# Performance work log

Hardware: AMD Instinct MI355X
Metric: run time of the kernel (lower is better)

Reference implementation:

```python
import jax, jax.numpy as jnp
import numpy as np

N, E, G = 20000, 320000, 64
IN_DIM, HID, HEADS, NCLS = 512, 256, 2, 10
EPS = 1e-5
SLOPE = 0.2


def setup_inputs() -> dict:
    key = jax.random.key(0)
    ks = jax.random.split(key, 24)
    s = 0.02
    inp = {
        "feat": jax.random.normal(ks[0], (N, IN_DIM), jnp.float32),
        "src": jax.random.randint(ks[1], (E,), 0, N, jnp.int32),
        "dst": jax.random.randint(ks[2], (E,), 0, N, jnp.int32),
        "graph_ids": jnp.sort(jax.random.randint(ks[3], (N,), 0, G, jnp.int32)),
        # GATv2Conv params (fc_src, fc_dst, attn)
        "W_src": jax.random.normal(ks[4], (IN_DIM, HEADS * HID), jnp.float32) * s,
        "b_src": jnp.zeros((HEADS * HID,), jnp.float32),
        "W_dst": jax.random.normal(ks[5], (IN_DIM, HEADS * HID), jnp.float32) * s,
        "b_dst": jnp.zeros((HEADS * HID,), jnp.float32),
        "attn": jax.random.normal(ks[6], (HEADS, HID), jnp.float32) * s,
        # skip_lin: input_dim -> 2*hidden
        "W_skip": jax.random.normal(ks[7], (IN_DIM, 2 * HID), jnp.float32) * s,
        "b_skip": jnp.zeros((2 * HID,), jnp.float32),
        # bn1 affine
        "gamma": jnp.ones((2 * HID,), jnp.float32),
        "beta": jnp.zeros((2 * HID,), jnp.float32),
        # dim_reducer
        "W_red": jax.random.normal(ks[8], (2 * HID, HID), jnp.float32) * s,
        "b_red": jnp.zeros((HID,), jnp.float32),
        # attention-pool gate Linear(hidden, 1)
        "w_gate": jax.random.normal(ks[9], (HID, 1), jnp.float32) * s,
        "b_gate": jnp.zeros((1,), jnp.float32),
        # classifier MLP
        "W1": jax.random.normal(ks[10], (HID, HID // 2), jnp.float32) * s,
        "b1": jnp.zeros((HID // 2,), jnp.float32),
        "W2": jax.random.normal(ks[11], (HID // 2, NCLS), jnp.float32) * s,
        "b2": jnp.zeros((NCLS,), jnp.float32),
    }
    return inp


def _gatv2(feat, src, dst, W_src, b_src, W_dst, b_dst, attn):
    # feat_src/feat_dst: [N, H, D]
    fs = (feat @ W_src + b_src).reshape(N, HEADS, HID)
    fd = (feat @ W_dst + b_dst).reshape(N, HEADS, HID)
    fs_e = fs[src]                               # [E, H, D]
    m = jax.nn.leaky_relu(fs_e + fd[dst], SLOPE)  # [E, H, D]
    e = jnp.einsum("ehd,hd->eh", m, attn)         # [E, H]
    # edge softmax grouped by destination node
    e_max = jax.ops.segment_max(e, dst, num_segments=N)          # [N, H]
    e_exp = jnp.exp(e - e_max[dst])                               # [E, H]
    denom = jax.ops.segment_sum(e_exp, dst, num_segments=N)      # [N, H]
    alpha = e_exp / denom[dst]                                    # [E, H]
    out = jax.ops.segment_sum(alpha[:, :, None] * fs_e, dst, num_segments=N)
    return out  # [N, H, D]; zero rows for zero in-degree nodes


def reference(feat, src, dst, graph_ids, W_src, b_src, W_dst, b_dst, attn,
              W_skip, b_skip, gamma, beta, W_red, b_red, w_gate, b_gate,
              W1, b1, W2, b2):
    h1 = jax.nn.elu(_gatv2(feat, src, dst, W_src, b_src, W_dst, b_dst, attn))
    h1 = h1.reshape(N, HEADS * HID)
    h1 = h1 + (feat @ W_skip + b_skip)
    # BatchNorm1d (training-mode batch statistics, biased variance)
    mu = jnp.mean(h1, axis=0)
    var = jnp.mean((h1 - mu) ** 2, axis=0)
    h1 = (h1 - mu) * jax.lax.rsqrt(var + EPS) * gamma + beta
    hr = h1 @ W_red + b_red                      # [N, HID]
    # GlobalAttentionPooling: segment softmax of gate scores over each graph
    gate = hr @ w_gate + b_gate                  # [N, 1]
    g_max = jax.ops.segment_max(gate, graph_ids, num_segments=G)
    g_exp = jnp.exp(gate - g_max[graph_ids])
    g_den = jax.ops.segment_sum(g_exp, graph_ids, num_segments=G)
    a = g_exp / g_den[graph_ids]                 # [N, 1]
    h_g = jax.ops.segment_sum(a * hr, graph_ids, num_segments=G)  # [G, HID]
    # classifier (dropout = identity at inference)
    return jax.nn.relu(h_g @ W1 + b1) @ W2 + b2  # [G, NCLS]
```

## Files before the change

kernel.cpp:

```cpp
#include <hip/hip_runtime.h>
#include <math.h>

#define N_NODES 20000
#define N_EDGES 320000
#define N_GRAPH 64
#define IN_DIM  512
#define HID     256
#define F2      512
#define EPS_BN  1e-5f
#define SLOPE   0.2f
#define SCAN_BLOCKS 79
#define N_RT    157
#define RT_PAD  20096

typedef unsigned short u16;
typedef __attribute__((ext_vector_type(8))) short bf16x8;
typedef __attribute__((ext_vector_type(4))) float floatx4;

__device__ __forceinline__ u16 bf_hi(float x) {
    unsigned int u = __float_as_uint(x);
    return (u16)((u + 0x7fffu + ((u >> 16) & 1u)) >> 16);
}
__device__ __forceinline__ float bf_val(u16 h) {
    return __uint_as_float((unsigned int)h << 16);
}
__device__ __forceinline__ void unpack2(unsigned int u, float& lo, float& hi) {
    lo = __uint_as_float(u << 16);
    hi = __uint_as_float(u & 0xffff0000u);
}
__device__ __forceinline__ float lr(float x) { return fmaxf(x, SLOPE * x); }

__global__ void init_zero_kernel(int* counts, int* cursor, float* stats,
                                 float* h_gnum, float* gden) {
    int i = blockIdx.x * blockDim.x + threadIdx.x;
    if (i < N_NODES) { counts[i] = 0; cursor[i] = 0; }
    if (i < 1024) stats[i] = 0.f;
    if (i < N_GRAPH * HID) h_gnum[i] = 0.f;
    if (i < N_GRAPH) gden[i] = 0.f;
}

__global__ __launch_bounds__(256) void split_feat_kernel(
    const float* __restrict__ X, u16* __restrict__ Hi, int total8, int pad8) {
    int i = blockIdx.x * 256 + threadIdx.x;
    if (i >= pad8) return;
    size_t base = (size_t)i * 8;
    if (i >= total8) {
        *(uint4*)(Hi + base) = make_uint4(0, 0, 0, 0);
        return;
    }
    float4 x0 = *(const float4*)(X + base);
    float4 x1 = *(const float4*)(X + base + 4);
    float xs[8] = {x0.x, x0.y, x0.z, x0.w, x1.x, x1.y, x1.z, x1.w};
    union { u16 s[8]; uint4 v; } h;
#pragma unroll
    for (int j = 0; j < 8; j++) h.s[j] = bf_hi(xs[j]);
    *(uint4*)(Hi + base) = h.v;
}

__global__ __launch_bounds__(256) void split_wt_kernel(
    const float* __restrict__ Ws, const float* __restrict__ Wd,
    const float* __restrict__ Wk, const float* __restrict__ Wr,
    u16* __restrict__ Hi, u16* __restrict__ Lo) {
    __shared__ float t[32][33];
    int w = blockIdx.z;
    int ncols = (w == 3) ? 256 : 512;
    int n0 = blockIdx.y * 32;
    if (n0 >= ncols) return;
    const float* W = (w == 0) ? Ws : ((w == 1) ? Wd : ((w == 2) ? Wk : Wr));
    size_t obase = (size_t)w * 512 * 512;
    int k0 = blockIdx.x * 32;
    int tx = threadIdx.x, ty = threadIdx.y;
#pragma unroll
    for (int i = 0; i < 4; i++)
        t[ty * 4 + i][tx] = W[(size_t)(k0 + ty * 4 + i) * ncols + n0 + tx];
    __syncthreads();
#pragma unroll
    for (int i = 0; i < 4; i++) {
        float x = t[tx][ty * 4 + i];
        u16 hh = bf_hi(x);
        size_t o = obase + (size_t)(n0 + ty * 4 + i) * 512 + k0 + tx;
        Hi[o] = hh;
        Lo[o] = bf_hi(x - bf_val(hh));
    }
}

__global__ __launch_bounds__(256) void gemm_mfma_triple(
    const u16* __restrict__ Fhi, const u16* __restrict__ Wthi,
    const float* __restrict__ b_src, const float* __restrict__ b_dst,
    const float* __restrict__ b_skip,
    u16* __restrict__ FS16, u16* __restrict__ FD16, float* __restrict__ h1) {
    __shared__ u16 As[2][128 * 72];
    int b = blockIdx.x;
    int xcd = b & 7, slot = b >> 3;
    int rt = (slot / 12) * 8 + xcd;
    if (rt >= N_RT) return;
    int cw = slot % 12;
    int w_idx = cw >> 2;
    int col0 = (cw & 3) * 128;
    int row0 = rt * 128;
    int tid = threadIdx.x;
    int lane = tid & 63, wave = tid >> 6;
    int wm = (wave & 1) * 64, wn = (wave >> 1) * 64;
    int quad = lane >> 4, l16 = lane & 15;

    int sr = tid >> 1, sh = (tid & 1) * 32;
    const u16* gA = Fhi + (size_t)(row0 + sr) * 512 + sh;
    int sOff = sr * 72 + sh;

    const u16* Wb = Wthi + (size_t)w_idx * 512 * 512;
    const u16* bP[4];
#pragma unroll
    for (int nt = 0; nt < 4; nt++)
        bP[nt] = Wb + (size_t)(col0 + wn + nt * 16 + l16) * 512 + quad * 8;

    floatx4 acc[4][4];
#pragma unroll
    for (int i = 0; i < 4; i++)
#pragma unroll
        for (int j = 0; j < 4; j++) acc[i][j] = (floatx4){0.f, 0.f, 0.f, 0.f};

    union { uint4 u; bf16x8 v; } bcur[8], bnxt[8];
    {
        uint4 a0 = *(const uint4*)(gA + 0);
        uint4 a1 = *(const uint4*)(gA + 8);
        uint4 a2 = *(const uint4*)(gA + 16);
        uint4 a3 = *(const uint4*)(gA + 24);
#pragma unroll
        for (int nt = 0; nt < 4; nt++) {
            bcur[nt * 2 + 0].u = *(const uint4*)(bP[nt] + 0);
            bcur[nt * 2 + 1].u = *(const uint4*)(bP[nt] + 32);
        }
        *(uint4*)(&As[0][sOff + 0])  = a0;
        *(uint4*)(&As[0][sOff + 8])  = a1;
        *(uint4*)(&As[0][sOff + 16]) = a2;
        *(uint4*)(&As[0][sOff + 24]) = a3;
    }
    __syncthreads();

    for (int kk = 0; kk < 8; kk++) {
        uint4 na0, na1, na2, na3;
        bool more = kk < 7;
        if (more) {
            int k1 = (kk + 1) * 64;
            na0 = *(const uint4*)(gA + k1 + 0);
            na1 = *(const uint4*)(gA + k1 + 8);
            na2 = *(const uint4*)(gA + k1 + 16);
            na3 = *(const uint4*)(gA + k1 + 24);
#pragma unroll
            for (int nt = 0; nt < 4; nt++) {
                bnxt[nt * 2 + 0].u = *(const uint4*)(bP[nt] + k1 + 0);
                bnxt[nt * 2 + 1].u = *(const uint4*)(bP[nt] + k1 + 32);
            }
        }
        const u16* base = &As[kk & 1][0];
#pragma unroll
        for (int s = 0; s < 2; s++) {
#pragma unroll
            for (int mt = 0; mt < 4; mt++) {
                bf16x8 ah = *(const bf16x8*)&base[(wm + mt * 16 + l16) * 72 + s * 32 + quad * 8];
#pragma unroll
                for (int nt = 0; nt < 4; nt++)
                    acc[mt][nt] = __builtin_amdgcn_mfma_f32_16x16x32_bf16(ah, bcur[nt * 2 + s].v, acc[mt][nt], 0, 0, 0);
            }
        }
        if (more) {
            u16* d = &As[(kk + 1) & 1][sOff];
            *(uint4*)(d + 0)  = na0;
            *(uint4*)(d + 8)  = na1;
            *(uint4*)(d + 16) = na2;
            *(uint4*)(d + 24) = na3;
            __syncthreads();
#pragma unroll
            for (int i = 0; i < 8; i++) bcur[i] = bnxt[i];
        }
    }

    const float* bias = (w_idx == 0) ? b_src : ((w_idx == 1) ? b_dst : b_skip);
    float bv[4];
#pragma unroll
    for (int nt = 0; nt < 4; nt++) bv[nt] = bias[col0 + wn + nt * 16 + l16];
#pragma unroll
    for (int mt = 0; mt < 4; mt++) {
#pragma unroll
        for (int r = 0; r < 4; r++) {
            int m = row0 + wm + mt * 16 + quad * 4 + r;
            if (m < N_NODES) {
#pragma unroll
                for (int nt = 0; nt < 4; nt++) {
                    int n = col0 + wn + nt * 16 + l16;
                    float vv = acc[mt][nt][r] + bv[nt];
                    if (w_idx == 0)      FS16[(size_t)m * 512 + n] = bf_hi(vv);
                    else if (w_idx == 1) FD16[(size_t)m * 512 + n] = bf_hi(vv);
                    else                 h1[(size_t)m * 512 + n] = vv;
                }
            }
        }
    }
}

__global__ __launch_bounds__(256) void gemm_mfma_red(
    const float* __restrict__ Af,
    const u16* __restrict__ Bhi, const u16* __restrict__ Blo,
    const float* __restrict__ bias, float* __restrict__ C,
    int Nrows, int M,
    const float* __restrict__ bscale, const float* __restrict__ bshift) {
    __shared__ u16 AsHi[128 * 40];
    __shared__ u16 AsLo[128 * 40];
    __shared__ float sBN[1024];
    int tid = threadIdx.x;
    int row0 = blockIdx.x * 128;
    int col0 = blockIdx.y * 128;
    int lane = tid & 63, wave = tid >> 6;
    int wm = (wave & 1) * 64, wn = (wave >> 1) * 64;
    int quad = lane >> 4, l16 = lane & 15;

    sBN[tid] = bscale[tid]; sBN[256 + tid] = bscale[256 + tid];
    sBN[512 + tid] = bshift[tid]; sBN[768 + tid] = bshift[256 + tid];
    __syncthreads();

    int sr = tid >> 1, sh = (tid & 1) * 16;
    int grow = row0 + sr;
    bool ok = grow < Nrows;
    u16* sA_hi = &AsHi[sr * 40 + sh];
    u16* sA_lo = &AsLo[sr * 40 + sh];

    floatx4 acc[4][4];
#pragma unroll
    for (int i = 0; i < 4; i++)
#pragma unroll
        for (int j = 0; j < 4; j++) acc[i][j] = (floatx4){0.f, 0.f, 0.f, 0.f};

    for (int k0 = 0; k0 < 512; k0 += 32) {
        float v[16];
        if (ok) {
            const float* g = Af + (size_t)grow * 512 + k0 + sh;
            *(float4*)&v[0]  = *(const float4*)(g);
            *(float4*)&v[4]  = *(const float4*)(g + 4);
            *(float4*)&v[8]  = *(const float4*)(g + 8);
            *(float4*)&v[12] = *(const float4*)(g + 12);
        } else {
#pragma unroll
            for (int j = 0; j < 16; j++) v[j] = 0.f;
        }
        union { u16 s[8]; uint4 u; } h0_, h1_, l0_, l1_;
#pragma unroll
        for (int j = 0; j < 16; j++) {
            int kc = k0 + sh + j;
            float x = v[j] * sBN[kc] + sBN[512 + kc];
            u16 hh = bf_hi(x);
            u16 ll = bf_hi(x - bf_val(hh));
            if (j < 8) { h0_.s[j] = hh; l0_.s[j] = ll; }
            else       { h1_.s[j - 8] = hh; l1_.s[j - 8] = ll; }
        }
        union { uint4 u; bf16x8 v; } bh[4], bl[4];
#pragma unroll
        for (int nt = 0; nt < 4; nt++) {
            size_t off = (size_t)(col0 + wn + nt * 16 + l16) * 512 + k0 + quad * 8;
            bh[nt].u = *(const uint4*)(Bhi + off);
            bl[nt].u = *(const uint4*)(Blo + off);
        }
        __syncthreads();
        *(uint4*)(sA_hi + 0) = h0_.u;
        *(uint4*)(sA_hi + 8) = h1_.u;
        *(uint4*)(sA_lo + 0) = l0_.u;
        *(uint4*)(sA_lo + 8) = l1_.u;
        __syncthreads();
#pragma unroll
        for (int mt = 0; mt < 4; mt++) {
            int me = (wm + mt * 16 + l16) * 40 + quad * 8;
            bf16x8 ah = *(const bf16x8*)&AsHi[me];
            bf16x8 al = *(const bf16x8*)&AsLo[me];
#pragma unroll
            for (int nt = 0; nt < 4; nt++) {
                acc[mt][nt] = __builtin_amdgcn_mfma_f32_16x16x32_bf16(ah, bh[nt].v, acc[mt][nt], 0, 0, 0);
                acc[mt][nt] = __builtin_amdgcn_mfma_f32_16x16x32_bf16(ah, bl[nt].v, acc[mt][nt], 0, 0, 0);
                acc[mt][nt] = __builtin_amdgcn_mfma_f32_16x16x32_bf16(al, bh[nt].v, acc[mt][nt], 0, 0, 0);
            }
        }
    }

    float bv[4];
#pragma unroll
    for (int nt = 0; nt < 4; nt++) bv[nt] = bias[col0 + wn + nt * 16 + l16];
#pragma unroll
    for (int mt = 0; mt < 4; mt++) {
#pragma unroll
        for (int r = 0; r < 4; r++) {
            int m = row0 + wm + mt * 16 + quad * 4 + r;
            if (m < Nrows) {
#pragma unroll
                for (int nt = 0; nt < 4; nt++) {
                    int n = col0 + wn + nt * 16 + l16;
                    C[(size_t)m * M + n] = acc[mt][nt][r] + bv[nt];
                }
            }
        }
    }
}

__global__ void hist_kernel(const int* __restrict__ dst, int* __restrict__ counts) {
    int e = blockIdx.x * blockDim.x + threadIdx.x;
    if (e < N_EDGES) atomicAdd(&counts[dst[e]], 1);
}

__global__ __launch_bounds__(256) void scan_local_kernel(
    const int* __restrict__ counts, int* __restrict__ row_ptr, int* __restrict__ bsum) {
    __shared__ int buf[256];
    int b = blockIdx.x, tid = threadIdx.x;
    int i = b * 256 + tid;
    buf[tid] = (i < N_NODES) ? counts[i] : 0;
    __syncthreads();
    for (int off = 1; off < 256; off <<= 1) {
        int t = (tid >= off) ? buf[tid - off] : 0;
        __syncthreads();
        buf[tid] += t;
        __syncthreads();
    }
    if (i < N_NODES) row_ptr[i + 1] = buf[tid];
    if (tid == 255) bsum[b] = buf[255];
}

__global__ __launch_bounds__(256) void scan_fixup_kernel(
    const int* __restrict__ bsum, int* __restrict__ row_ptr) {
    __shared__ int red[256];
    int b = blockIdx.x, tid = threadIdx.x;
    red[tid] = (tid < b) ? bsum[tid] : 0;
    __syncthreads();
    for (int off = 128; off > 0; off >>= 1) {
        if (tid < off) red[tid] += red[tid + off];
        __syncthreads();
    }
    int offset = red[0];
    int i = b * 256 + tid;
    if (i < N_NODES) row_ptr[i + 1] += offset;
    if (b == 0 && tid == 0) row_ptr[0] = 0;
}

__global__ void scatter_kernel(const int* __restrict__ src, const int* __restrict__ dst,
                               const int* __restrict__ row_ptr,
                               int* __restrict__ cursor, int* __restrict__ csr_src) {
    int e = blockIdx.x * blockDim.x + threadIdx.x;
    if (e < N_EDGES) {
        int d = dst[e];
        int pos = atomicAdd(&cursor[d], 1);
        csr_src[row_ptr[d] + pos] = src[e];
    }
}

__global__ __launch_bounds__(256) void edge_fused_kernel(
    const u16* __restrict__ FS16, const u16* __restrict__ FD16,
    const float* __restrict__ attn, const int* __restrict__ csr_src,
    const int* __restrict__ row_ptr, float* __restrict__ h1) {
    __shared__ float red[3 * 512];
    __shared__ float den[2];
    int n = blockIdx.x, tid = threadIdx.x;
    int lane = tid & 63, wave = tid >> 6;
    int beg = row_ptr[n], end = row_ptr[n + 1], deg = end - beg;
    if (tid < 2) den[tid] = 0.f;

    float fdv[8], aw[8];
    {
        uint4 q = *(const uint4*)(FD16 + (size_t)n * 512 + 8 * lane);
        unpack2(q.x, fdv[0], fdv[1]); unpack2(q.y, fdv[2], fdv[3]);
        unpack2(q.z, fdv[4], fdv[5]); unpack2(q.w, fdv[6], fdv[7]);
        float4 a0 = *(const float4*)(attn + 8 * lane);
        float4 a1 = *(const float4*)(attn + 8 * lane + 4);
        aw[0] = a0.x; aw[1] = a0.y; aw[2] = a0.z; aw[3] = a0.w;
        aw[4] = a1.x; aw[5] = a1.y; aw[6] = a1.z; aw[7] = a1.w;
    }
    __syncthreads();

    float acc[8] = {0.f, 0.f, 0.f, 0.f, 0.f, 0.f, 0.f, 0.f};
    float dp = 0.f;
    for (int j = wave; j < deg; j += 4) {
        int s = csr_src[beg + j];
        uint4 q = *(const uint4*)(FS16 + (size_t)s * 512 + 8 * lane);
        float f[8];
        unpack2(q.x, f[0], f[1]); unpack2(q.y, f[2], f[3]);
        unpack2(q.z, f[4], f[5]); unpack2(q.w, f[6], f[7]);
        float p = 0.f;
#pragma unroll
        for (int k = 0; k < 8; k++) p += lr(f[k] + fdv[k]) * aw[k];
#pragma unroll
        for (int off = 16; off > 0; off >>= 1) p += __shfl_xor(p, off, 64);
        float ex = expf(p);
#pragma unroll
        for (int k = 0; k < 8; k++) acc[k] += ex * f[k];
        if ((lane & 31) == 0) dp += ex;
    }
    if ((lane & 31) == 0) atomicAdd(&den[lane >> 5], dp);

    if (wave > 0) {
        float* r = &red[(wave - 1) * 512 + lane * 8];
        *(float4*)(r + 0) = *(float4*)&acc[0];
        *(float4*)(r + 4) = *(float4*)&acc[4];
    }
    __syncthreads();
    if (wave == 0) {
#pragma unroll
        for (int w = 0; w < 3; w++) {
            const float* r = &red[w * 512 + lane * 8];
#pragma unroll
            for (int k = 0; k < 8; k++) acc[k] += r[k];
        }
        float d = (lane < 32) ? den[0] : den[1];
        float inv = d > 0.f ? 1.f / d : 0.f;
        float* hp = h1 + (size_t)n * 512 + 8 * lane;
        float4 s0 = *(float4*)(hp);
        float4 s1 = *(float4*)(hp + 4);
        float v[8];
#pragma unroll
        for (int k = 0; k < 8; k++) {
            float x = acc[k] * inv;
            v[k] = x > 0.f ? x : expm1f(x);
        }
        s0.x += v[0]; s0.y += v[1]; s0.z += v[2]; s0.w += v[3];
        s1.x += v[4]; s1.y += v[5]; s1.z += v[6]; s1.w += v[7];
        *(float4*)(hp) = s0;
        *(float4*)(hp + 4) = s1;
    }
}

__global__ __launch_bounds__(256) void bn_stats_kernel(const float* __restrict__ h1,
                                                       float* __restrict__ stats,
                                                       int rows_per_block) {
    int tid = threadIdx.x;
    int r0 = blockIdx.x * rows_per_block;
    int r1 = min(r0 + rows_per_block, N_NODES);
    float s0 = 0.f, q0 = 0.f, s1 = 0.f, q1 = 0.f;
    for (int r = r0; r < r1; r++) {
        float a = h1[(size_t)r * F2 + tid];
        float b = h1[(size_t)r * F2 + 256 + tid];
        s0 += a; q0 += a * a;
        s1 += b; q1 += b * b;
    }
    atomicAdd(&stats[tid], s0);
    atomicAdd(&stats[256 + tid], s1);
    atomicAdd(&stats[512 + tid], q0);
    atomicAdd(&stats[512 + 256 + tid], q1);
}

__global__ void bn_finalize_kernel(const float* __restrict__ stats,
                                   const float* __restrict__ gamma,
                                   const float* __restrict__ beta,
                                   float* __restrict__ bscale, float* __restrict__ bshift) {
    int c = threadIdx.x;
    float mu = stats[c] / (float)N_NODES;
    float var = stats[512 + c] / (float)N_NODES - mu * mu;
    float sc = gamma[c] * rsqrtf(var + EPS_BN);
    bscale[c] = sc;
    bshift[c] = beta[c] - mu * sc;
}

__global__ __launch_bounds__(256) void gate_kernel(const float* __restrict__ hr,
                                                   const float* __restrict__ wg,
                                                   float* __restrict__ gate) {
    int n = blockIdx.x * 4 + (threadIdx.x >> 6);
    int lane = threadIdx.x & 63;
    const float4* row = (const float4*)(hr + (size_t)n * HID);
    const float4* w = (const float4*)wg;
    float4 a = row[lane], b = w[lane];
    float p = a.x * b.x + a.y * b.y + a.z * b.z + a.w * b.w;
#pragma unroll
    for (int off = 32; off > 0; off >>= 1) p += __shfl_down(p, off, 64);
    if (lane == 0) gate[n] = p;
}

__device__ __forceinline__ int lower_bound_dev(const int* a, int n, int v) {
    int lo = 0, hi = n;
    while (lo < hi) {
        int mid = (lo + hi) >> 1;
        if (a[mid] < v) lo = mid + 1; else hi = mid;
    }
    return lo;
}

__global__ __launch_bounds__(256) void pool_partial_kernel(
    const float* __restrict__ hr, const float* __restrict__ gate,
    const int* __restrict__ gids, float* __restrict__ h_gnum,
    float* __restrict__ gden) {
    int b = blockIdx.x;
    int g = b >> 3, part = b & 7;
    int tid = threadIdx.x;
    int start = lower_bound_dev(gids, N_NODES, g);
    int end = lower_bound_dev(gids, N_NODES, g + 1);
    int span = end - start;
    int p_beg = start + (span * part) / 8;
    int p_end = start + (span * (part + 1)) / 8;
    if (p_beg >= p_end) return;
    __shared__ float wa[256];
    __shared__ float red[256];
    float acc = 0.f, denacc = 0.f;
    for (int cbeg = p_beg; cbeg < p_end; cbeg += 256) {
        int c = min(256, p_end - cbeg);
        float e = 0.f;
        if (tid < c) { e = expf(gate[cbeg + tid]); wa[tid] = e; }
        red[tid] = (tid < c) ? e : 0.f;
        __syncthreads();
        for (int off = 128; off > 0; off >>= 1) {
            if (tid < off) red[tid] += red[tid + off];
            __syncthreads();
        }
        denacc += red[0];
        for (int i = 0; i < c; i++) acc += wa[i] * hr[(size_t)(cbeg + i) * HID + tid];
        __syncthreads();
    }
    atomicAdd(&h_gnum[g * HID + tid], acc);
    if (tid == 0) atomicAdd(&gden[g], denacc);
}

__global__ __launch_bounds__(128) void classifier_kernel(
    const float* __restrict__ h_gnum, const float* __restrict__ gden,
    const float* __restrict__ W1, const float* __restrict__ b1,
    const float* __restrict__ W2, const float* __restrict__ b2,
    float* __restrict__ out) {
    int g = blockIdx.x;
    int tid = threadIdx.x;
    __shared__ float hg[256];
    __shared__ float z1[128];
    float d = gden[g];
    float invd = d > 0.f ? 1.f / d : 0.f;
    hg[tid] = h_gnum[g * HID + tid] * invd;
    hg[tid + 128] = h_gnum[g * HID + tid + 128] * invd;
    __syncthreads();
    float a = b1[tid];
#pragma unroll 8
    for (int k = 0; k < 256; k++) a += hg[k] * W1[k * 128 + tid];
    z1[tid] = a > 0.f ? a : 0.f;
    __syncthreads();
    if (tid < 10) {
        float o = b2[tid];
#pragma unroll 8
        for (int j = 0; j < 128; j++) o += z1[j] * W2[j * 10 + tid];
        out[g * 10 + tid] = o;
    }
}

extern "C" void kernel_launch(void* const* d_in, const int* in_sizes, int n_in,
                              void* d_out, int out_size, void* d_ws, size_t ws_size,
                              hipStream_t stream) {
    const float* feat   = (const float*)d_in[0];
    const int*   src    = (const int*)d_in[1];
    const int*   dst    = (const int*)d_in[2];
    const int*   gids   = (const int*)d_in[3];
    const float* W_src  = (const float*)d_in[4];
    const float* b_src  = (const float*)d_in[5];
    const float* W_dst  = (const float*)d_in[6];
    const float* b_dst  = (const float*)d_in[7];
    const float* attn   = (const float*)d_in[8];
    const float* W_skip = (const float*)d_in[9];
    const float* b_skip = (const float*)d_in[10];
    const float* gamma  = (const float*)d_in[11];
    const float* beta   = (const float*)d_in[12];
    const float* W_red  = (const float*)d_in[13];
    const float* b_red  = (const float*)d_in[14];
    const float* w_gate = (const float*)d_in[15];
    const float* W1     = (const float*)d_in[17];
    const float* b1     = (const float*)d_in[18];
    const float* W2     = (const float*)d_in[19];
    const float* b2     = (const float*)d_in[20];
    float* out = (float*)d_out;

    char* p = (char*)d_ws;
    auto alloc = [&](size_t bytes) -> char* {
        char* r = p;
        p += (bytes + 255) & ~(size_t)255;
        return r;
    };
    u16*   FS16     = (u16*)alloc((size_t)N_NODES * F2 * 2);
    u16*   FD16     = (u16*)alloc((size_t)N_NODES * F2 * 2);
    float* h1       = (float*)alloc((size_t)N_NODES * F2 * 4);
    float* gate     = (float*)alloc((size_t)N_NODES * 4);
    float* stats    = (float*)alloc(1024 * 4);
    float* bn_scale = (float*)alloc(512 * 4);
    float* bn_shift = (float*)alloc(512 * 4);
    float* h_gnum   = (float*)alloc((size_t)N_GRAPH * HID * 4);
    float* gden     = (float*)alloc((size_t)N_GRAPH * 4);
    int* counts     = (int*)alloc((size_t)N_NODES * 4);
    int* row_ptr    = (int*)alloc((size_t)(N_NODES + 1) * 4);
    int* cursor     = (int*)alloc((size_t)N_NODES * 4);
    int* csr_src    = (int*)alloc((size_t)N_EDGES * 4);
    int* bsum       = (int*)alloc((size_t)SCAN_BLOCKS * 4);
    u16* Fhi        = (u16*)alloc((size_t)RT_PAD * IN_DIM * 2);
    u16* Wthi       = (u16*)alloc((size_t)4 * 512 * 512 * 2);
    u16* Wtlo       = (u16*)alloc((size_t)4 * 512 * 512 * 2);
    float* hr = (float*)Fhi;
    (void)ws_size; (void)in_sizes; (void)n_in; (void)out_size;

    const size_t WSZ = (size_t)512 * 512;

    init_zero_kernel<<<(N_NODES + 255) / 256, 256, 0, stream>>>(counts, cursor, stats, h_gnum, gden);
    split_feat_kernel<<<(RT_PAD * IN_DIM / 8 + 255) / 256, 256, 0, stream>>>(
        feat, Fhi, N_NODES * IN_DIM / 8, RT_PAD * IN_DIM / 8);
    split_wt_kernel<<<dim3(16, 16, 4), dim3(32, 8), 0, stream>>>(
        W_src, W_dst, W_skip, W_red, Wthi, Wtlo);

    gemm_mfma_triple<<<dim3(((N_RT + 7) / 8) * 8 * 12), 256, 0, stream>>>(
        Fhi, Wthi, b_src, b_dst, b_skip, FS16, FD16, h1);

    hist_kernel<<<(N_EDGES + 255) / 256, 256, 0, stream>>>(dst, counts);
    scan_local_kernel<<<SCAN_BLOCKS, 256, 0, stream>>>(counts, row_ptr, bsum);
    scan_fixup_kernel<<<SCAN_BLOCKS, 256, 0, stream>>>(bsum, row_ptr);
    scatter_kernel<<<(N_EDGES + 255) / 256, 256, 0, stream>>>(src, dst, row_ptr, cursor, csr_src);

    edge_fused_kernel<<<N_NODES, 256, 0, stream>>>(FS16, FD16, attn, csr_src, row_ptr, h1);

    bn_stats_kernel<<<500, 256, 0, stream>>>(h1, stats, 40);
    bn_finalize_kernel<<<1, 512, 0, stream>>>(stats, gamma, beta, bn_scale, bn_shift);

    dim3 g256((N_NODES + 127) / 128, 2);
    gemm_mfma_red<<<g256, 256, 0, stream>>>(
        h1, Wthi + 3 * WSZ, Wtlo + 3 * WSZ, b_red, hr, N_NODES, HID,
        bn_scale, bn_shift);

    gate_kernel<<<N_NODES / 4, 256, 0, stream>>>(hr, w_gate, gate);

    pool_partial_kernel<<<N_GRAPH * 8, 256, 0, stream>>>(hr, gate, gids, h_gnum, gden);

    classifier_kernel<<<N_GRAPH, 128, 0, stream>>>(h_gnum, gden, W1, b1, W2, b2, out);
}
```

Before: 423.5 us.

## Store h1 as bf16 hi/lo pairs, fold BN into W_red, fuse gate into GEMM

The skip/h1 buffer is now kept as split bf16 hi/lo halves instead of fp32, and the edge kernel does its read-modify-write in that format. BatchNorm scale and shift are folded into the reduction weights and bias by a new small kernel, so the reduction GEMM loads pre-split A tiles with no per-element conversion. The gate dot product moves into the GEMM epilogue through shuffles and atomics, which removes one kernel and a reread of hr. BN statistics are computed from the hi half only, which slightly lowers their precision.

```diff
diff --git a/kernel.cpp b/kernel.cpp
--- a/kernel.cpp
+++ b/kernel.cpp
@@ -31,9 +31,9 @@
 __device__ __forceinline__ float lr(float x) { return fmaxf(x, SLOPE * x); }
 
 __global__ void init_zero_kernel(int* counts, int* cursor, float* stats,
-                                 float* h_gnum, float* gden) {
+                                 float* h_gnum, float* gden, float* gate) {
     int i = blockIdx.x * blockDim.x + threadIdx.x;
-    if (i < N_NODES) { counts[i] = 0; cursor[i] = 0; }
+    if (i < N_NODES) { counts[i] = 0; cursor[i] = 0; gate[i] = 0.f; }
     if (i < 1024) stats[i] = 0.f;
     if (i < N_GRAPH * HID) h_gnum[i] = 0.f;
     if (i < N_GRAPH) gden[i] = 0.f;
@@ -88,7 +88,8 @@
     const u16* __restrict__ Fhi, const u16* __restrict__ Wthi,
     const float* __restrict__ b_src, const float* __restrict__ b_dst,
     const float* __restrict__ b_skip,
-    u16* __restrict__ FS16, u16* __restrict__ FD16, float* __restrict__ h1) {
+    u16* __restrict__ FS16, u16* __restrict__ FD16,
+    u16* __restrict__ h1hi, u16* __restrict__ h1lo) {
     __shared__ u16 As[2][128 * 72];
     int b = blockIdx.x;
     int xcd = b & 7, slot = b >> 3;
@@ -191,107 +192,11 @@
                     float vv = acc[mt][nt][r] + bv[nt];
                     if (w_idx == 0)      FS16[(size_t)m * 512 + n] = bf_hi(vv);
                     else if (w_idx == 1) FD16[(size_t)m * 512 + n] = bf_hi(vv);
-                    else                 h1[(size_t)m * 512 + n] = vv;
-                }
-            }
-        }
-    }
-}
-
-__global__ __launch_bounds__(256) void gemm_mfma_red(
-    const float* __restrict__ Af,
-    const u16* __restrict__ Bhi, const u16* __restrict__ Blo,
-    const float* __restrict__ bias, float* __restrict__ C,
-    int Nrows, int M,
-    const float* __restrict__ bscale, const float* __restrict__ bshift) {
-    __shared__ u16 AsHi[128 * 40];
-    __shared__ u16 AsLo[128 * 40];
-    __shared__ float sBN[1024];
-    int tid = threadIdx.x;
-    int row0 = blockIdx.x * 128;
-    int col0 = blockIdx.y * 128;
-    int lane = tid & 63, wave = tid >> 6;
-    int wm = (wave & 1) * 64, wn = (wave >> 1) * 64;
-    int quad = lane >> 4, l16 = lane & 15;
-
-    sBN[tid] = bscale[tid]; sBN[256 + tid] = bscale[256 + tid];
-    sBN[512 + tid] = bshift[tid]; sBN[768 + tid] = bshift[256 + tid];
-    __syncthreads();
-
-    int sr = tid >> 1, sh = (tid & 1) * 16;
-    int grow = row0 + sr;
-    bool ok = grow < Nrows;
-    u16* sA_hi = &AsHi[sr * 40 + sh];
-    u16* sA_lo = &AsLo[sr * 40 + sh];
-
-    floatx4 acc[4][4];
-#pragma unroll
-    for (int i = 0; i < 4; i++)
-#pragma unroll
-        for (int j = 0; j < 4; j++) acc[i][j] = (floatx4){0.f, 0.f, 0.f, 0.f};
-
-    for (int k0 = 0; k0 < 512; k0 += 32) {
-        float v[16];
-        if (ok) {
-            const float* g = Af + (size_t)grow * 512 + k0 + sh;
-            *(float4*)&v[0]  = *(const float4*)(g);
-            *(float4*)&v[4]  = *(const float4*)(g + 4);
-            *(float4*)&v[8]  = *(const float4*)(g + 8);
-            *(float4*)&v[12] = *(const float4*)(g + 12);
-        } else {
-#pragma unroll
-            for (int j = 0; j < 16; j++) v[j] = 0.f;
-        }
-        union { u16 s[8]; uint4 u; } h0_, h1_, l0_, l1_;
-#pragma unroll
-        for (int j = 0; j < 16; j++) {
-            int kc = k0 + sh + j;
-            float x = v[j] * sBN[kc] + sBN[512 + kc];
-            u16 hh = bf_hi(x);
-            u16 ll = bf_hi(x - bf_val(hh));
-            if (j < 8) { h0_.s[j] = hh; l0_.s[j] = ll; }
-            else       { h1_.s[j - 8] = hh; l1_.s[j - 8] = ll; }
-        }
-        union { uint4 u; bf16x8 v; } bh[4], bl[4];
-#pragma unroll
-        for (int nt = 0; nt < 4; nt++) {
-            size_t off = (size_t)(col0 + wn + nt * 16 + l16) * 512 + k0 + quad * 8;
-            bh[nt].u = *(const uint4*)(Bhi + off);
-            bl[nt].u = *(const uint4*)(Blo + off);
-        }
-        __syncthreads();
-        *(uint4*)(sA_hi + 0) = h0_.u;
-        *(uint4*)(sA_hi + 8) = h1_.u;
-        *(uint4*)(sA_lo + 0) = l0_.u;
-        *(uint4*)(sA_lo + 8) = l1_.u;
-        __syncthreads();
-#pragma unroll
-        for (int mt = 0; mt < 4; mt++) {
-            int me = (wm + mt * 16 + l16) * 40 + quad * 8;
-            bf16x8 ah = *(const bf16x8*)&AsHi[me];
-            bf16x8 al = *(const bf16x8*)&AsLo[me];
-#pragma unroll
-            for (int nt = 0; nt < 4; nt++) {
-                acc[mt][nt] = __builtin_amdgcn_mfma_f32_16x16x32_bf16(ah, bh[nt].v, acc[mt][nt], 0, 0, 0);
-                acc[mt][nt] = __builtin_amdgcn_mfma_f32_16x16x32_bf16(ah, bl[nt].v, acc[mt][nt], 0, 0, 0);
-                acc[mt][nt] = __builtin_amdgcn_mfma_f32_16x16x32_bf16(al, bh[nt].v, acc[mt][nt], 0, 0, 0);
-            }
-        }
-    }
-
-    float bv[4];
-#pragma unroll
-    for (int nt = 0; nt < 4; nt++) bv[nt] = bias[col0 + wn + nt * 16 + l16];
-#pragma unroll
-    for (int mt = 0; mt < 4; mt++) {
-#pragma unroll
-        for (int r = 0; r < 4; r++) {
-            int m = row0 + wm + mt * 16 + quad * 4 + r;
-            if (m < Nrows) {
-#pragma unroll
-                for (int nt = 0; nt < 4; nt++) {
-                    int n = col0 + wn + nt * 16 + l16;
-                    C[(size_t)m * M + n] = acc[mt][nt][r] + bv[nt];
+                    else {
+                        u16 hh = bf_hi(vv);
+                        h1hi[(size_t)m * 512 + n] = hh;
+                        h1lo[(size_t)m * 512 + n] = bf_hi(vv - bf_val(hh));
+                    }
                 }
             }
         }
@@ -350,7 +255,8 @@
 __global__ __launch_bounds__(256) void edge_fused_kernel(
     const u16* __restrict__ FS16, const u16* __restrict__ FD16,
     const float* __restrict__ attn, const int* __restrict__ csr_src,
-    const int* __restrict__ row_ptr, float* __restrict__ h1) {
+    const int* __restrict__ row_ptr,
+    u16* __restrict__ h1hi, u16* __restrict__ h1lo) {
     __shared__ float red[3 * 512];
     __shared__ float den[2];
     int n = blockIdx.x, tid = threadIdx.x;
@@ -405,23 +311,26 @@
         }
         float d = (lane < 32) ? den[0] : den[1];
         float inv = d > 0.f ? 1.f / d : 0.f;
-        float* hp = h1 + (size_t)n * 512 + 8 * lane;
-        float4 s0 = *(float4*)(hp);
-        float4 s1 = *(float4*)(hp + 4);
-        float v[8];
+        size_t base = (size_t)n * 512 + 8 * lane;
+        union { u16 s[8]; uint4 v; } qh, ql;
+        qh.v = *(const uint4*)(h1hi + base);
+        ql.v = *(const uint4*)(h1lo + base);
 #pragma unroll
         for (int k = 0; k < 8; k++) {
+            float skip = bf_val(qh.s[k]) + bf_val(ql.s[k]);
             float x = acc[k] * inv;
-            v[k] = x > 0.f ? x : expm1f(x);
-        }
-        s0.x += v[0]; s0.y += v[1]; s0.z += v[2]; s0.w += v[3];
-        s1.x += v[4]; s1.y += v[5]; s1.z += v[6]; s1.w += v[7];
-        *(float4*)(hp) = s0;
-        *(float4*)(hp + 4) = s1;
-    }
-}
-
-__global__ __launch_bounds__(256) void bn_stats_kernel(const float* __restrict__ h1,
+            x = x > 0.f ? x : expm1f(x);
+            float y = x + skip;
+            u16 hh = bf_hi(y);
+            qh.s[k] = hh;
+            ql.s[k] = bf_hi(y - bf_val(hh));
+        }
+        *(uint4*)(h1hi + base) = qh.v;
+        *(uint4*)(h1lo + base) = ql.v;
+    }
+}
+
+__global__ __launch_bounds__(256) void bn_stats_kernel(const u16* __restrict__ h1hi,
                                                        float* __restrict__ stats,
                                                        int rows_per_block) {
     int tid = threadIdx.x;
@@ -429,8 +338,8 @@
     int r1 = min(r0 + rows_per_block, N_NODES);
     float s0 = 0.f, q0 = 0.f, s1 = 0.f, q1 = 0.f;
     for (int r = r0; r < r1; r++) {
-        float a = h1[(size_t)r * F2 + tid];
-        float b = h1[(size_t)r * F2 + 256 + tid];
+        float a = bf_val(h1hi[(size_t)r * F2 + tid]);
+        float b = bf_val(h1hi[(size_t)r * F2 + 256 + tid]);
         s0 += a; q0 += a * a;
         s1 += b; q1 += b * b;
     }
@@ -452,18 +361,130 @@
     bshift[c] = beta[c] - mu * sc;
 }
 
-__global__ __launch_bounds__(256) void gate_kernel(const float* __restrict__ hr,
-                                                   const float* __restrict__ wg,
-                                                   float* __restrict__ gate) {
-    int n = blockIdx.x * 4 + (threadIdx.x >> 6);
-    int lane = threadIdx.x & 63;
-    const float4* row = (const float4*)(hr + (size_t)n * HID);
-    const float4* w = (const float4*)wg;
-    float4 a = row[lane], b = w[lane];
-    float p = a.x * b.x + a.y * b.y + a.z * b.z + a.w * b.w;
-#pragma unroll
-    for (int off = 32; off > 0; off >>= 1) p += __shfl_down(p, off, 64);
-    if (lane == 0) gate[n] = p;
+__global__ __launch_bounds__(256) void bn_fold_kernel(
+    const u16* __restrict__ Whi3, const u16* __restrict__ Wlo3,
+    const float* __restrict__ bscale, const float* __restrict__ bshift,
+    const float* __restrict__ b_red,
+    u16* __restrict__ Wphi, u16* __restrict__ Wplo, float* __restrict__ bias2) {
+    __shared__ float red[256];
+    int n = blockIdx.x, tid = threadIdx.x;
+    float part = 0.f;
+    for (int k = tid; k < 512; k += 256) {
+        size_t o = (size_t)n * 512 + k;
+        float w = bf_val(Whi3[o]) + bf_val(Wlo3[o]);
+        part += bshift[k] * w;
+        float wp = w * bscale[k];
+        u16 hh = bf_hi(wp);
+        Wphi[o] = hh;
+        Wplo[o] = bf_hi(wp - bf_val(hh));
+    }
+    red[tid] = part; __syncthreads();
+    for (int off = 128; off > 0; off >>= 1) {
+        if (tid < off) red[tid] += red[tid + off];
+        __syncthreads();
+    }
+    if (tid == 0) bias2[n] = b_red[n] + red[0];
+}
+
+__global__ __launch_bounds__(256) void gemm_mfma_red(
+    const u16* __restrict__ Ahi, const u16* __restrict__ Alo,
+    const u16* __restrict__ Bhi, const u16* __restrict__ Blo,
+    const float* __restrict__ bias2, const float* __restrict__ wg,
+    float* __restrict__ hr, float* __restrict__ gate) {
+    __shared__ u16 AsHi[128 * 40];
+    __shared__ u16 AsLo[128 * 40];
+    int tid = threadIdx.x;
+    int row0 = blockIdx.x * 128;
+    int col0 = blockIdx.y * 128;
+    int lane = tid & 63, wave = tid >> 6;
+    int wm = (wave & 1) * 64, wn = (wave >> 1) * 64;
+    int quad = lane >> 4, l16 = lane & 15;
+
+    int sr = tid >> 1, sh = (tid & 1) * 16;
+    int grow = row0 + sr;
+    bool ok = grow < N_NODES;
+    u16* sH = &AsHi[sr * 40 + sh];
+    u16* sL = &AsLo[sr * 40 + sh];
+
+    const u16* bPh[4];
+    const u16* bPl[4];
+#pragma unroll
+    for (int nt = 0; nt < 4; nt++) {
+        size_t o = (size_t)(col0 + wn + nt * 16 + l16) * 512 + quad * 8;
+        bPh[nt] = Bhi + o;
+        bPl[nt] = Blo + o;
+    }
+
+    floatx4 acc[4][4];
+#pragma unroll
+    for (int i = 0; i < 4; i++)
+#pragma unroll
+        for (int j = 0; j < 4; j++) acc[i][j] = (floatx4){0.f, 0.f, 0.f, 0.f};
+
+    for (int k0 = 0; k0 < 512; k0 += 32) {
+        uint4 h0 = make_uint4(0, 0, 0, 0), h1v = h0, l0 = h0, l1 = h0;
+        if (ok) {
+            const u16* g = Ahi + (size_t)grow * 512 + k0 + sh;
+            const u16* gl = Alo + (size_t)grow * 512 + k0 + sh;
+            h0 = *(const uint4*)(g);
+            h1v = *(const uint4*)(g + 8);
+            l0 = *(const uint4*)(gl);
+            l1 = *(const uint4*)(gl + 8);
+        }
+        union { uint4 u; bf16x8 v; } bh[4], bl[4];
+#pragma unroll
+        for (int nt = 0; nt < 4; nt++) {
+            bh[nt].u = *(const uint4*)(bPh[nt] + k0);
+            bl[nt].u = *(const uint4*)(bPl[nt] + k0);
+        }
+        __syncthreads();
+        *(uint4*)(sH + 0) = h0;
+        *(uint4*)(sH + 8) = h1v;
+        *(uint4*)(sL + 0) = l0;
+        *(uint4*)(sL + 8) = l1;
+        __syncthreads();
+#pragma unroll
+        for (int mt = 0; mt < 4; mt++) {
+            int me = (wm + mt * 16 + l16) * 40 + quad * 8;
+            bf16x8 ah = *(const bf16x8*)&AsHi[me];
+            bf16x8 al = *(const bf16x8*)&AsLo[me];
+#pragma unroll
+            for (int nt = 0; nt < 4; nt++) {
+                acc[mt][nt] = __builtin_amdgcn_mfma_f32_16x16x32_bf16(ah, bh[nt].v, acc[mt][nt], 0, 0, 0);
+                acc[mt][nt] = __builtin_amdgcn_mfma_f32_16x16x32_bf16(ah, bl[nt].v, acc[mt][nt], 0, 0, 0);
+                acc[mt][nt] = __builtin_amdgcn_mfma_f32_16x16x32_bf16(al, bh[nt].v, acc[mt][nt], 0, 0, 0);
+            }
+        }
+    }
+
+    float bv[4], wgv[4];
+#pragma unroll
+    for (int nt = 0; nt < 4; nt++) {
+        int n = col0 + wn + nt * 16 + l16;
+        bv[nt] = bias2[n];
+        wgv[nt] = wg[n];
+    }
+#pragma unroll
+    for (int mt = 0; mt < 4; mt++) {
+#pragma unroll
+        for (int r = 0; r < 4; r++) {
+            int m = row0 + wm + mt * 16 + quad * 4 + r;
+            float vv[4], g = 0.f;
+#pragma unroll
+            for (int nt = 0; nt < 4; nt++) {
+                vv[nt] = acc[mt][nt][r] + bv[nt];
+                g += vv[nt] * wgv[nt];
+            }
+#pragma unroll
+            for (int s = 8; s > 0; s >>= 1) g += __shfl_xor(g, s, 64);
+            if (m < N_NODES) {
+#pragma unroll
+                for (int nt = 0; nt < 4; nt++)
+                    hr[(size_t)m * HID + col0 + wn + nt * 16 + l16] = vv[nt];
+                if (l16 == 0) atomicAdd(&gate[m], g);
+            }
+        }
+    }
 }
 
 __device__ __forceinline__ int lower_bound_dev(const int* a, int n, int v) {
@@ -569,11 +590,13 @@
     };
     u16*   FS16     = (u16*)alloc((size_t)N_NODES * F2 * 2);
     u16*   FD16     = (u16*)alloc((size_t)N_NODES * F2 * 2);
-    float* h1       = (float*)alloc((size_t)N_NODES * F2 * 4);
+    u16*   h1hi     = (u16*)alloc((size_t)N_NODES * F2 * 2);
+    u16*   h1lo     = (u16*)alloc((size_t)N_NODES * F2 * 2);
     float* gate     = (float*)alloc((size_t)N_NODES * 4);
     float* stats    = (float*)alloc(1024 * 4);
     float* bn_scale = (float*)alloc(512 * 4);
     float* bn_shift = (float*)alloc(512 * 4);
+    float* bias2    = (float*)alloc(256 * 4);
     float* h_gnum   = (float*)alloc((size_t)N_GRAPH * HID * 4);
     float* gden     = (float*)alloc((size_t)N_GRAPH * 4);
     int* counts     = (int*)alloc((size_t)N_NODES * 4);
@@ -584,36 +607,39 @@
     u16* Fhi        = (u16*)alloc((size_t)RT_PAD * IN_DIM * 2);
     u16* Wthi       = (u16*)alloc((size_t)4 * 512 * 512 * 2);
     u16* Wtlo       = (u16*)alloc((size_t)4 * 512 * 512 * 2);
+    u16* Wphi       = (u16*)alloc((size_t)HID * 512 * 2);
+    u16* Wplo       = (u16*)alloc((size_t)HID * 512 * 2);
     float* hr = (float*)Fhi;
     (void)ws_size; (void)in_sizes; (void)n_in; (void)out_size;
 
     const size_t WSZ = (size_t)512 * 512;
 
-    init_zero_kernel<<<(N_NODES + 255) / 256, 256, 0, stream>>>(counts, cursor, stats, h_gnum, gden);
+    init_zero_kernel<<<(N_NODES + 255) / 256, 256, 0, stream>>>(
+        counts, cursor, stats, h_gnum, gden, gate);
     split_feat_kernel<<<(RT_PAD * IN_DIM / 8 + 255) / 256, 256, 0, stream>>>(
         feat, Fhi, N_NODES * IN_DIM / 8, RT_PAD * IN_DIM / 8);
     split_wt_kernel<<<dim3(16, 16, 4), dim3(32, 8), 0, stream>>>(
         W_src, W_dst, W_skip, W_red, Wthi, Wtlo);
 
     gemm_mfma_triple<<<dim3(((N_RT + 7) / 8) * 8 * 12), 256, 0, stream>>>(
-        Fhi, Wthi, b_src, b_dst, b_skip, FS16, FD16, h1);
+        Fhi, Wthi, b_src, b_dst, b_skip, FS16, FD16, h1hi, h1lo);
 
     hist_kernel<<<(N_EDGES + 255) / 256, 256, 0, stream>>>(dst, counts);
     scan_local_kernel<<<SCAN_BLOCKS, 256, 0, stream>>>(counts, row_ptr, bsum);
     scan_fixup_kernel<<<SCAN_BLOCKS, 256, 0, stream>>>(bsum, row_ptr);
     scatter_kernel<<<(N_EDGES + 255) / 256, 256, 0, stream>>>(src, dst, row_ptr, cursor, csr_src);
 
-    edge_fused_kernel<<<N_NODES, 256, 0, stream>>>(FS16, FD16, attn, csr_src, row_ptr, h1);
-
-    bn_stats_kernel<<<500, 256, 0, stream>>>(h1, stats, 40);
+    edge_fused_kernel<<<N_NODES, 256, 0, stream>>>(
+        FS16, FD16, attn, csr_src, row_ptr, h1hi, h1lo);
+
+    bn_stats_kernel<<<500, 256, 0, stream>>>(h1hi, stats, 40);
     bn_finalize_kernel<<<1, 512, 0, stream>>>(stats, gamma, beta, bn_scale, bn_shift);
+    bn_fold_kernel<<<HID, 256, 0, stream>>>(
+        Wthi + 3 * WSZ, Wtlo + 3 * WSZ, bn_scale, bn_shift, b_red, Wphi, Wplo, bias2);
 
     dim3 g256((N_NODES + 127) / 128, 2);
     gemm_mfma_red<<<g256, 256, 0, stream>>>(
-        h1, Wthi + 3 * WSZ, Wtlo + 3 * WSZ, b_red, hr, N_NODES, HID,
-        bn_scale, bn_shift);
-
-    gate_kernel<<<N_NODES / 4, 256, 0, stream>>>(hr, w_gate, gate);
+        h1hi, h1lo, Wphi, Wplo, bias2, w_gate, hr, gate);
 
     pool_partial_kernel<<<N_GRAPH * 8, 256, 0, stream>>>(hr, gate, gids, h_gnum, gden);
 
```

New measurement: 433.2 us. 1.02x slower.
